# Kernel optimization log

Measured on AMD Instinct MI355X. Metric: run time of the kernel, lower is better.

## Reference

```python
import jax, jax.numpy as jnp
import numpy as np

VOCAB = 21
EPS = 1e-5


def rmsnorm(x, w):
    return x * jax.lax.rsqrt(jnp.mean(x * x, axis=-1, keepdims=True) + EPS) * w


def mamba_layer(h, in_w, conv_w, conv_b, xp_w, dtp_w, dtp_b, A_log, Dp, out_w):
    # h: (B, L, D)
    Bsz, L, _ = h.shape
    di, dc = conv_w.shape
    n = A_log.shape[-1]
    r = dtp_w.shape[-1]
    xz = jnp.einsum('bld,ed->ble', h, in_w)          # (B, L, 2*di)
    xi, z = jnp.split(xz, 2, axis=-1)
    # causal depthwise conv of width dc
    xp = jnp.pad(xi, ((0, 0), (dc - 1, 0), (0, 0)))
    xc = conv_b + sum(xp[:, k:k + L, :] * conv_w[:, k] for k in range(dc))
    xc = jax.nn.silu(xc)                              # (B, L, di)
    dbc = jnp.einsum('bld,ed->ble', xc, xp_w)         # (B, L, r+2n)
    dt, Bm, Cm = dbc[..., :r], dbc[..., r:r + n], dbc[..., r + n:]
    dt = jax.nn.softplus(jnp.einsum('blr,dr->bld', dt, dtp_w) + dtp_b)  # (B, L, di)
    A = -jnp.exp(A_log)                               # (di, n)

    def step(hst, inp):
        x_t, dt_t, B_t, C_t = inp                     # (B,di),(B,di),(B,n),(B,n)
        dA = jnp.exp(dt_t[..., None] * A)             # (B, di, n)
        hst = dA * hst + (dt_t * x_t)[..., None] * B_t[:, None, :]
        y_t = jnp.einsum('bdn,bn->bd', hst, C_t)
        return hst, y_t

    h0 = jnp.zeros((Bsz, di, n), dtype=h.dtype)
    xs = (xc.swapaxes(0, 1), dt.swapaxes(0, 1), Bm.swapaxes(0, 1), Cm.swapaxes(0, 1))
    _, ys = jax.lax.scan(step, h0, xs)
    y = ys.swapaxes(0, 1) + xc * Dp                   # skip term D*x
    y = y * jax.nn.silu(z)                            # gate
    return jnp.einsum('bld,ed->ble', y, out_w)


def setup_inputs() -> dict:
    key = jax.random.key(0)
    B, L, D = 4, 1024, 512
    n_layers, n, dc, expand = 2, 16, 3, 2
    di = expand * D
    r = (D + 15) // 16  # dt_rank = ceil(d_model/16) = 32
    ks = jax.random.split(key, 12)
    f32 = jnp.float32
    inp = {}
    inp['x'] = jax.random.randint(ks[0], (B, L), 0, VOCAB)
    inp['emb'] = 0.02 * jax.random.normal(ks[1], (VOCAB, D), f32)
    inp['norm_w'] = jnp.ones((n_layers, D), f32)
    inp['in_proj_w'] = (D ** -0.5) * jax.random.normal(ks[2], (n_layers, 2 * di, D), f32)
    inp['conv_w'] = (dc ** -0.5) * jax.random.normal(ks[3], (n_layers, di, dc), f32)
    inp['conv_b'] = jnp.zeros((n_layers, di), f32)
    inp['x_proj_w'] = (di ** -0.5) * jax.random.normal(ks[4], (n_layers, r + 2 * n, di), f32)
    inp['dt_proj_w'] = (r ** -0.5) * jax.random.normal(ks[5], (n_layers, di, r), f32)
    inp['dt_proj_b'] = jax.random.uniform(ks[6], (n_layers, di), f32, minval=-4.0, maxval=-1.0)
    inp['A_log'] = jnp.log(jnp.broadcast_to(jnp.arange(1, n + 1, dtype=f32), (n_layers, di, n)))
    inp['D_param'] = jnp.ones((n_layers, di), f32)
    inp['out_proj_w'] = (di ** -0.5) * jax.random.normal(ks[7], (n_layers, D, di), f32)
    inp['fc_w'] = (D ** -0.5) * jax.random.normal(ks[8], (2, D), f32)
    inp['fc_b'] = jnp.zeros((2,), f32)
    return inp


def reference(x, emb, norm_w, in_proj_w, conv_w, conv_b, x_proj_w, dt_proj_w,
              dt_proj_b, A_log, D_param, out_proj_w, fc_w, fc_b):
    h = emb[x].astype(jnp.float32)                    # (B, L, D)
    n_layers = norm_w.shape[0]
    for l in range(n_layers):
        h = rmsnorm(
            mamba_layer(h, in_proj_w[l], conv_w[l], conv_b[l], x_proj_w[l],
                        dt_proj_w[l], dt_proj_b[l], A_log[l], D_param[l],
                        out_proj_w[l]),
            norm_w[l])
    pooled = jnp.mean(h, axis=1)                      # global_pool=True
    out = jnp.tanh(pooled)                            # dropout is identity at eval
    return out @ fc_w.T + fc_b                        # (B, 2)
```

## Files before the change

### kernel.cpp

```cpp
#include <hip/hip_runtime.h>
#include <math.h>

constexpr int Bsz = 4, Lseq = 1024, Dmodel = 512, NLAYERS = 2;
constexpr int DI = 1024, NST = 16, RNK = 32;
constexpr int BLQ = Bsz * Lseq;
constexpr int NCH = 32, CLEN = 32;

typedef __attribute__((ext_vector_type(8))) short short8v;
typedef __attribute__((ext_vector_type(8))) unsigned short ushort8v;
typedef __attribute__((ext_vector_type(4))) float f32x4;
typedef unsigned short ushort;

__device__ inline ushort bf16_rne(float v) {
  unsigned u = __float_as_uint(v);
  u += 0x7FFFu + ((u >> 16) & 1u);
  return (ushort)(u >> 16);
}
__device__ inline float bf2f(ushort u) {
  return __uint_as_float(((unsigned)u) << 16);
}
__device__ inline size_t frag_off(int row, int k, int KT) {
  int kt = k >> 6, kk = (k >> 5) & 1, k8 = (k >> 3) & 3;
  int lanei = (row & 15) | (k8 << 4), msub = (row >> 4) & 7, rt = row >> 7;
  return ((((size_t)(rt * KT + kt) * 2 + kk) * 8 + msub) * 64 + lanei) * 8;
}
#define GLDS(gp, lp) __builtin_amdgcn_global_load_lds( \
    (const __attribute__((address_space(1))) void*)(gp), \
    (__attribute__((address_space(3))) void*)(lp), 16, 0, 0)

__global__ __launch_bounds__(256) void embcvt_kernel(
    const int* __restrict__ x, const float* __restrict__ emb,
    const float* __restrict__ in_w, const float* __restrict__ xp_w,
    const float* __restrict__ out_w,
    ushort* __restrict__ Af,
    ushort* __restrict__ WIh, ushort* __restrict__ WIl,
    ushort* __restrict__ XPh, ushort* __restrict__ XPl,
    ushort* __restrict__ WOh)
{
  int blk = blockIdx.x;
  if (blk < 1024) {
    int i = blk * 256 + threadIdx.x;
    int row = i >> 6, k = (i & 63) * 8;
    int tok = x[row];
    const float* src = &emb[(size_t)tok * Dmodel + k];
    float4 v0 = *reinterpret_cast<const float4*>(src);
    float4 v1 = *reinterpret_cast<const float4*>(src + 4);
    float xs[8] = {v0.x, v0.y, v0.z, v0.w, v1.x, v1.y, v1.z, v1.w};
    ushort hv[8];
#pragma unroll
    for (int e = 0; e < 8; ++e) hv[e] = bf16_rne(xs[e]);
    *reinterpret_cast<ushort8v*>(&Af[frag_off(row, k, 8)]) =
        *reinterpret_cast<ushort8v*>(hv);
    return;
  }
  const float* src; ushort *dh, *dl; size_t doff; bool wantlo = true;
  if (blk < 2048) {
    int u = (blk - 1024) * 256 + threadIdx.x;
    int l = u >> 17, rem = u & 131071;
    int row = rem >> 6, k = (rem & 63) * 8;
    src = in_w + (size_t)l * 2048 * 512 + (size_t)row * 512 + k;
    size_t base = (size_t)l * 2048 * 512;
    dh = WIh + base; dl = WIl + base; doff = frag_off(row, k, 8);
  } else if (blk < 2112) {
    int u = (blk - 2048) * 256 + threadIdx.x;
    int l = u >> 13, rem = u & 8191;
    int row = rem >> 7, k = (rem & 127) * 8;
    src = xp_w + (size_t)l * 64 * 1024 + (size_t)row * 1024 + k;
    size_t base = (size_t)l * 131072;
    dh = XPh + base; dl = XPl + base; doff = frag_off(row, k, 16);
  } else {
    int u = (blk - 2112) * 256 + threadIdx.x;
    int l = u >> 16, rem = u & 65535;
    int row = rem >> 7, k = (rem & 127) * 8;
    src = out_w + (size_t)l * 512 * 1024 + (size_t)row * 1024 + k;
    size_t base = (size_t)l * 512 * 1024;
    dh = WOh + base; dl = nullptr; doff = frag_off(row, k, 16); wantlo = false;
  }
  float4 v0 = *reinterpret_cast<const float4*>(src);
  float4 v1 = *reinterpret_cast<const float4*>(src + 4);
  float xs[8] = {v0.x, v0.y, v0.z, v0.w, v1.x, v1.y, v1.z, v1.w};
  ushort hs[8], ls[8];
#pragma unroll
  for (int j = 0; j < 8; ++j) {
    unsigned u = __float_as_uint(xs[j]);
    float hf = __uint_as_float(u & 0xFFFF0000u);
    float r = xs[j] - hf;
    hs[j] = (ushort)(u >> 16);
    ls[j] = (ushort)(__float_as_uint(r) >> 16);
  }
  *reinterpret_cast<ushort8v*>(&dh[doff]) = *reinterpret_cast<ushort8v*>(hs);
  if (wantlo)
    *reinterpret_cast<ushort8v*>(&dl[doff]) = *reinterpret_cast<ushort8v*>(ls);
}

__global__ __launch_bounds__(256) void gemm_in_mfma(
    const ushort* __restrict__ Ah,
    const ushort* __restrict__ Bh, const ushort* __restrict__ Bl,
    ushort* __restrict__ C)
{
  extern __shared__ ushort smu[];
  constexpr int AOFF = 0, BHOFF = 4096, BLOFF = 20480;
  const int tid = threadIdx.x, lane = tid & 63, wid = tid >> 6;
  const int bn = blockIdx.x, bm = blockIdx.y;
  const int bm0 = bm * 64;
  const int rtA = bm0 >> 7, half = (bm0 >> 6) & 1;
  f32x4 acc[4][4];
#pragma unroll
  for (int i = 0; i < 4; ++i)
#pragma unroll
    for (int j = 0; j < 4; ++j) acc[i][j] = (f32x4){0.f, 0.f, 0.f, 0.f};
  const int rtB = wid >> 1;
  const int nsub = (wid & 1) * 4;

  for (int kt = 0; kt < 8; ++kt) {
    if (wid == 0) {
      const ushort* cb = Ah + ((size_t)(rtA * 8 + kt)) * 8192;
#pragma unroll
      for (int kk = 0; kk < 2; ++kk)
#pragma unroll
        for (int m = 0; m < 4; ++m)
          GLDS(cb + (kk * 8 + half * 4 + m) * 512 + lane * 8,
               smu + AOFF + (kk * 4 + m) * 512);
    } else if (wid == 1) {
#pragma unroll
      for (int rt = 0; rt < 2; ++rt) {
        const ushort* cb = Bh + ((size_t)((bn * 2 + rt) * 8 + kt)) * 8192;
#pragma unroll
        for (int i = 0; i < 16; ++i)
          GLDS(cb + i * 512 + lane * 8, smu + BHOFF + rt * 8192 + i * 512);
      }
    } else if (wid == 2) {
#pragma unroll
      for (int rt = 0; rt < 2; ++rt) {
        const ushort* cb = Bl + ((size_t)((bn * 2 + rt) * 8 + kt)) * 8192;
#pragma unroll
        for (int i = 0; i < 16; ++i)
          GLDS(cb + i * 512 + lane * 8, smu + BLOFF + rt * 8192 + i * 512);
      }
    }
    __syncthreads();
#pragma unroll
    for (int kk = 0; kk < 2; ++kk) {
      short8v a[4], b[4];
#pragma unroll
      for (int i = 0; i < 4; ++i)
        a[i] = *reinterpret_cast<const short8v*>(&smu[AOFF + ((kk * 4 + i) * 64 + lane) * 8]);
#pragma unroll
      for (int j = 0; j < 4; ++j)
        b[j] = *reinterpret_cast<const short8v*>(
            &smu[BHOFF + rtB * 8192 + ((kk * 8 + nsub + j) * 64 + lane) * 8]);
#pragma unroll
      for (int ms = 0; ms < 4; ++ms)
#pragma unroll
        for (int ns = 0; ns < 4; ++ns)
          acc[ms][ns] = __builtin_amdgcn_mfma_f32_16x16x32_bf16(a[ms], b[ns], acc[ms][ns], 0, 0, 0);
#pragma unroll
      for (int j = 0; j < 4; ++j)
        b[j] = *reinterpret_cast<const short8v*>(
            &smu[BLOFF + rtB * 8192 + ((kk * 8 + nsub + j) * 64 + lane) * 8]);
#pragma unroll
      for (int ms = 0; ms < 4; ++ms)
#pragma unroll
        for (int ns = 0; ns < 4; ++ns)
          acc[ms][ns] = __builtin_amdgcn_mfma_f32_16x16x32_bf16(a[ms], b[ns], acc[ms][ns], 0, 0, 0);
    }
    __syncthreads();
  }
  const int cr = lane >> 4, cc = lane & 15;
#pragma unroll
  for (int ms = 0; ms < 4; ++ms) {
    int row0 = bm0 + ms * 16 + cr * 4;
#pragma unroll
    for (int ns = 0; ns < 4; ++ns) {
      int col = bn * 256 + wid * 64 + ns * 16 + cc;
#pragma unroll
      for (int r = 0; r < 4; ++r)
        C[(size_t)(row0 + r) * 2048 + col] = bf16_rne(acc[ms][ns][r]);
    }
  }
}

__global__ __launch_bounds__(256) void gemm_out_mfma(
    const ushort* __restrict__ Ah, const ushort* __restrict__ Bh,
    float* __restrict__ P)
{
  constexpr int ASZ = 8192;
  __shared__ ushort lds[2 * ASZ];
  const int tid = threadIdx.x, lane = tid & 63, wid = tid >> 6;
  const int wm = wid >> 1, wn = wid & 1;
  const int bm = blockIdx.y, bn = blockIdx.x, z = blockIdx.z;
  f32x4 acc[4][4];
#pragma unroll
  for (int i = 0; i < 4; ++i)
#pragma unroll
    for (int j = 0; j < 4; ++j) acc[i][j] = (f32x4){0.f, 0.f, 0.f, 0.f};
  const int msel = wm * 4, nsel = wn * 4;
  for (int kt = z * 4; kt < z * 4 + 4; ++kt) {
    if (wid == 0) {
      const ushort* cb = Ah + ((size_t)(bm * 16 + kt)) * 8192;
#pragma unroll
      for (int i = 0; i < 16; ++i)
        GLDS(cb + i * 512 + lane * 8, lds + i * 512);
    } else if (wid == 1) {
      const ushort* cb = Bh + ((size_t)(bn * 16 + kt)) * 8192;
#pragma unroll
      for (int i = 0; i < 16; ++i)
        GLDS(cb + i * 512 + lane * 8, lds + ASZ + i * 512);
    }
    __syncthreads();
#pragma unroll
    for (int kk = 0; kk < 2; ++kk) {
      short8v a[4], b[4];
#pragma unroll
      for (int i = 0; i < 4; ++i) {
        a[i] = *reinterpret_cast<const short8v*>(&lds[((kk * 8 + msel + i) * 64 + lane) * 8]);
        b[i] = *reinterpret_cast<const short8v*>(&lds[ASZ + ((kk * 8 + nsel + i) * 64 + lane) * 8]);
      }
#pragma unroll
      for (int ms = 0; ms < 4; ++ms)
#pragma unroll
        for (int ns = 0; ns < 4; ++ns)
          acc[ms][ns] = __builtin_amdgcn_mfma_f32_16x16x32_bf16(a[ms], b[ns], acc[ms][ns], 0, 0, 0);
    }
    __syncthreads();
  }
  float* Pz = P + (size_t)z * BLQ * Dmodel;
  const int cr = lane >> 4, cc = lane & 15;
#pragma unroll
  for (int ms = 0; ms < 4; ++ms) {
    int row0 = bm * 128 + (msel + ms) * 16 + cr * 4;
#pragma unroll
    for (int ns = 0; ns < 4; ++ns) {
      int col = bn * 128 + (nsel + ns) * 16 + cc;
#pragma unroll
      for (int r = 0; r < 4; ++r)
        Pz[(size_t)(row0 + r) * Dmodel + col] = acc[ms][ns][r];
    }
  }
}

__global__ __launch_bounds__(256) void convxp_kernel(
    const ushort* __restrict__ XZb, const float* __restrict__ cw,
    const float* __restrict__ cb,
    const ushort* __restrict__ XPh, const ushort* __restrict__ XPl,
    float* __restrict__ XC, float* __restrict__ P)
{
  constexpr int XZOFF = 0;
  constexpr int AOFF  = 1312;
  constexpr int BHOFF = 2336;
  constexpr int BLOFF = 6432;
  __shared__ ushort smu[10528];
  const int tid = threadIdx.x, lane = tid & 63, wid = tid >> 6;
  const int cr = lane >> 4, cc = lane & 15;
  const int bm0 = blockIdx.x * 16;
  const int z = blockIdx.y;
  const int batchbase = bm0 & ~(Lseq - 1);
  f32x4 acc = (f32x4){0.f, 0.f, 0.f, 0.f};

  for (int kt = z * 4; kt < z * 4 + 4; ++kt) {
    const int kcol0 = kt * 64;
    if (wid < 2) {
#pragma unroll
      for (int i = 0; i < 2; ++i) {
        int u = tid + i * 128;
        if (u < 144) {
          int r = u >> 3, c8 = u & 7;
          int grow = bm0 - 2 + r;
          ushort8v v = {};
          if (grow >= batchbase)
            v = *reinterpret_cast<const ushort8v*>(
                &XZb[(size_t)grow * 2048 + kcol0 + c8 * 8]);
          *reinterpret_cast<ushort8v*>(&smu[XZOFF + r * 72 + c8 * 8]) = v;
        }
      }
    } else {
      const ushort* src = ((wid == 2) ? XPh : XPl) + (size_t)kt * 8192 + lane * 8;
      int dst0 = (wid == 2) ? BHOFF : BLOFF;
#pragma unroll
      for (int i = 0; i < 8; ++i) {
        int sidx = (i >> 2) * 8 + (i & 3);
        GLDS(src + sidx * 512, smu + dst0 + i * 512);
      }
    }
    __syncthreads();
    if (tid < 128) {
      int row = tid >> 3, c8 = tid & 7;
      int d0 = kcol0 + c8 * 8;
      ushort8v cur = *reinterpret_cast<ushort8v*>(&smu[XZOFF + (row + 2) * 72 + c8 * 8]);
      ushort8v pm1 = *reinterpret_cast<ushort8v*>(&smu[XZOFF + (row + 1) * 72 + c8 * 8]);
      ushort8v pm2 = *reinterpret_cast<ushort8v*>(&smu[XZOFF + (row + 0) * 72 + c8 * 8]);
      float wv[24], bv[8];
#pragma unroll
      for (int q = 0; q < 6; ++q)
        *reinterpret_cast<float4*>(&wv[q * 4]) =
            *reinterpret_cast<const float4*>(&cw[d0 * 3 + q * 4]);
      *reinterpret_cast<float4*>(&bv[0]) = *reinterpret_cast<const float4*>(&cb[d0]);
      *reinterpret_cast<float4*>(&bv[4]) = *reinterpret_cast<const float4*>(&cb[d0 + 4]);
      float os[8]; ushort hv[8];
#pragma unroll
      for (int e = 0; e < 8; ++e) {
        float a = bv[e];
        a = fmaf(bf2f(pm2[e]), wv[e * 3 + 0], a);
        a = fmaf(bf2f(pm1[e]), wv[e * 3 + 1], a);
        a = fmaf(bf2f(cur[e]), wv[e * 3 + 2], a);
        float s = a / (1.f + __expf(-a));
        os[e] = s; hv[e] = bf16_rne(s);
      }
      float* op = &XC[(size_t)(bm0 + row) * DI + d0];
      *reinterpret_cast<float4*>(op) = *reinterpret_cast<float4*>(&os[0]);
      *reinterpret_cast<float4*>(op + 4) = *reinterpret_cast<float4*>(&os[4]);
      int kk = c8 >> 2, k8 = c8 & 3;
      int idx = (kk * 64 + (row | (k8 << 4))) ^ k8;
      *reinterpret_cast<ushort8v*>(&smu[AOFF + idx * 8]) =
          *reinterpret_cast<ushort8v*>(hv);
    }
    __syncthreads();
#pragma unroll
    for (int kk = 0; kk < 2; ++kk) {
      int aidx = (kk * 64 + lane) ^ ((lane >> 4) & 3);
      short8v a = *reinterpret_cast<const short8v*>(&smu[AOFF + aidx * 8]);
      short8v bh = *reinterpret_cast<const short8v*>(&smu[BHOFF + ((kk * 4 + wid) * 64 + lane) * 8]);
      short8v bl = *reinterpret_cast<const short8v*>(&smu[BLOFF + ((kk * 4 + wid) * 64 + lane) * 8]);
      acc = __builtin_amdgcn_mfma_f32_16x16x32_bf16(a, bh, acc, 0, 0, 0);
      acc = __builtin_amdgcn_mfma_f32_16x16x32_bf16(a, bl, acc, 0, 0, 0);
    }
    __syncthreads();
  }
  float* Pz = P + (size_t)z * BLQ * 64;
#pragma unroll
  for (int r = 0; r < 4; ++r)
    Pz[(size_t)(bm0 + cr * 4 + r) * 64 + wid * 16 + cc] = acc[r];
}

__global__ __launch_bounds__(256) void xpost_kernel(
    const float* __restrict__ P, const float* __restrict__ dtw,
    const float* __restrict__ dtb, float* __restrict__ DTb,
    float* __restrict__ BCc)
{
  const int tid = threadIdx.x;
  const size_t SL = (size_t)BLQ * 64;
  if (blockIdx.y == 16) {
    int i0 = blockIdx.x * 4096 + tid;
#pragma unroll
    for (int i = 0; i < 16; ++i) {
      int idx = i0 + i * 256;
      int bt = idx >> 5, n = idx & 31;
      size_t g = (size_t)bt * 64 + 32 + n;
      BCc[idx] = (P[g] + P[SL + g]) + (P[2 * SL + g] + P[3 * SL + g]);
    }
    return;
  }
  const int dg = blockIdx.y, bm0 = blockIdx.x * 128;
  __shared__ float db[128][33];
  __shared__ float wt[64][33];
#pragma unroll
  for (int i = 0; i < 16; ++i) {
    int e = tid + i * 256;
    int r = e >> 5, c = e & 31;
    size_t g = (size_t)(bm0 + r) * 64 + c;
    db[r][c] = (P[g] + P[SL + g]) + (P[2 * SL + g] + P[3 * SL + g]);
  }
#pragma unroll
  for (int i = 0; i < 8; ++i) {
    int e = tid + i * 256;
    int r = e >> 5, c = e & 31;
    wt[r][c] = dtw[(size_t)(dg * 64 + r) * 32 + c];
  }
  __syncthreads();
  const int d_loc = tid & 63, wv = tid >> 6;
  const float bias = dtb[dg * 64 + d_loc];
#pragma unroll 4
  for (int i = 0; i < 32; ++i) {
    int r = wv + i * 4;
    float dot = 0.f;
#pragma unroll
    for (int c = 0; c < 32; ++c) dot = fmaf(db[r][c], wt[d_loc][c], dot);
    float v = dot + bias;
    DTb[(size_t)(bm0 + r) * DI + dg * 64 + d_loc] =
        (v > 15.f) ? v : log1pf(__expf(v));
  }
}

__global__ __launch_bounds__(256) void scan_p1_kernel(
    const float* __restrict__ DTb, const float* __restrict__ XC,
    const float* __restrict__ BCc, const float* __restrict__ Alog,
    float* __restrict__ HEND, float* __restrict__ DSUM)
{
  const int d = blockIdx.x * 256 + threadIdx.x;
  const int c = blockIdx.y, b = blockIdx.z;
  const int t0 = b * Lseq + c * CLEN;
  __shared__ float Bs[CLEN][16];
#pragma unroll
  for (int i = 0; i < 2; ++i) {
    int e = threadIdx.x + i * 256;
    Bs[e >> 4][e & 15] = BCc[(size_t)(t0 + (e >> 4)) * 32 + (e & 15)];
  }
  float An[16];
#pragma unroll
  for (int j = 0; j < 4; ++j) {
    float4 a = *reinterpret_cast<const float4*>(&Alog[d * 16 + j * 4]);
    An[j * 4 + 0] = -__expf(a.x); An[j * 4 + 1] = -__expf(a.y);
    An[j * 4 + 2] = -__expf(a.z); An[j * 4 + 3] = -__expf(a.w);
  }
  __syncthreads();
  float h[16] = {};
  float S = 0.f;
  for (int t = 0; t < CLEN; ++t) {
    size_t g = (size_t)(t0 + t) * DI + d;
    float dt = DTb[g], xc = XC[g];
    S += dt;
    float dtxc = dt * xc;
#pragma unroll
    for (int n = 0; n < 16; ++n)
      h[n] = fmaf(__expf(An[n] * dt), h[n], dtxc * Bs[t][n]);
  }
  size_t hb = ((size_t)(b * NCH + c) * DI + d) * 16;
#pragma unroll
  for (int j = 0; j < 4; ++j)
    *reinterpret_cast<float4*>(&HEND[hb + j * 4]) =
        *reinterpret_cast<float4*>(&h[j * 4]);
  DSUM[(size_t)(b * NCH + c) * DI + d] = S;
}

__global__ __launch_bounds__(256) void scan_p2_kernel(
    float* __restrict__ HEND, const float* __restrict__ DSUM,
    const float* __restrict__ Alog)
{
  int id = blockIdx.x * 256 + threadIdx.x;
  int n = id & 15, d = (id >> 4) & (DI - 1), b = id >> 14;
  float An = -__expf(Alog[d * 16 + n]);
  float hg = 0.f;
  for (int c = 0; c < NCH; ++c) {
    size_t hi = ((size_t)(b * NCH + c) * DI + d) * 16 + n;
    float hl = HEND[hi];
    float Dc = DSUM[(size_t)(b * NCH + c) * DI + d];
    HEND[hi] = hg;
    hg = fmaf(__expf(An * Dc), hg, hl);
  }
}

__global__ __launch_bounds__(256) void scan_p3_kernel(
    const float* __restrict__ XC, const float* __restrict__ DTb,
    const float* __restrict__ BCc, const ushort* __restrict__ XZb,
    const float* __restrict__ HEND, const float* __restrict__ Alog,
    const float* __restrict__ Dp, ushort* __restrict__ Af)
{
  const int tid = threadIdx.x;
  const int dg = blockIdx.x, c = blockIdx.y, b = blockIdx.z;
  const int d = dg * 256 + tid;
  const int t0 = b * Lseq + c * CLEN;
  __shared__ float BC[CLEN][32];
  __shared__ float ys[CLEN][264];
#pragma unroll
  for (int i = 0; i < 4; ++i) {
    int e = tid + i * 256;
    BC[e >> 5][e & 31] = BCc[(size_t)(t0 + (e >> 5)) * 32 + (e & 31)];
  }
  float An[16], h[16];
  size_t hb = ((size_t)(b * NCH + c) * DI + d) * 16;
#pragma unroll
  for (int j = 0; j < 4; ++j) {
    float4 a = *reinterpret_cast<const float4*>(&Alog[d * 16 + j * 4]);
    An[j * 4 + 0] = -__expf(a.x); An[j * 4 + 1] = -__expf(a.y);
    An[j * 4 + 2] = -__expf(a.z); An[j * 4 + 3] = -__expf(a.w);
    *reinterpret_cast<float4*>(&h[j * 4]) =
        *reinterpret_cast<const float4*>(&HEND[hb + j * 4]);
  }
  float Dpv = Dp[d];
  __syncthreads();
  for (int t = 0; t < CLEN; ++t) {
    size_t g = (size_t)(t0 + t) * DI + d;
    float dt = DTb[g], xc = XC[g];
    float z = bf2f(XZb[(size_t)(t0 + t) * (2 * DI) + DI + d]);
    float dtxc = dt * xc;
    float y = 0.f;
#pragma unroll
    for (int n = 0; n < 16; ++n) {
      h[n] = fmaf(__expf(An[n] * dt), h[n], dtxc * BC[t][n]);
      y = fmaf(h[n], BC[t][16 + n], y);
    }
    float sil = z / (1.f + __expf(-z));
    ys[t][tid] = (y + xc * Dpv) * sil;
  }
  __syncthreads();
#pragma unroll
  for (int i = 0; i < 4; ++i) {
    int u = tid + i * 256;
    int tt = u >> 5, j8 = u & 31;
    int row = t0 + tt;
    int kg = dg * 256 + j8 * 8;
    ushort hv[8];
#pragma unroll
    for (int e = 0; e < 8; ++e) hv[e] = bf16_rne(ys[tt][j8 * 8 + e]);
    *reinterpret_cast<ushort8v*>(&Af[frag_off(row, kg, 16)]) =
        *reinterpret_cast<ushort8v*>(hv);
  }
}

template<int LAST>
__global__ __launch_bounds__(256) void rmsnorm_kernel(const float* __restrict__ X,
    const float* __restrict__ W, ushort* __restrict__ Af, float* __restrict__ PP) {
  __shared__ float pr[4][512];
  int w = threadIdx.x >> 6, lane = threadIdx.x & 63;
  int row = blockIdx.x * 4 + w;
  int k = lane * 8;
  const size_t SL = (size_t)BLQ * Dmodel;
  size_t idx = (size_t)row * Dmodel + k;
  float vs[8];
#pragma unroll
  for (int h = 0; h < 2; ++h) {
    float4 a = *reinterpret_cast<const float4*>(&X[idx + h * 4]);
    float4 b = *reinterpret_cast<const float4*>(&X[SL + idx + h * 4]);
    float4 c = *reinterpret_cast<const float4*>(&X[2 * SL + idx + h * 4]);
    float4 d = *reinterpret_cast<const float4*>(&X[3 * SL + idx + h * 4]);
    vs[h * 4 + 0] = (a.x + b.x) + (c.x + d.x);
    vs[h * 4 + 1] = (a.y + b.y) + (c.y + d.y);
    vs[h * 4 + 2] = (a.z + b.z) + (c.z + d.z);
    vs[h * 4 + 3] = (a.w + b.w) + (c.w + d.w);
  }
  float ss = 0.f;
#pragma unroll
  for (int e = 0; e < 8; ++e) ss = fmaf(vs[e], vs[e], ss);
#pragma unroll
  for (int o = 32; o >= 1; o >>= 1) ss += __shfl_xor(ss, o);
  float sc = rsqrtf(ss * (1.f / Dmodel) + 1e-5f);
  const float* wp = W + k;
  float4 w0 = *reinterpret_cast<const float4*>(wp);
  float4 w1 = *reinterpret_cast<const float4*>(wp + 4);
  float wsv[8] = {w0.x, w0.y, w0.z, w0.w, w1.x, w1.y, w1.z, w1.w};
  float os[8];
#pragma unroll
  for (int e = 0; e < 8; ++e) os[e] = vs[e] * sc * wsv[e];
  if (LAST == 0) {
    ushort hv[8];
#pragma unroll
    for (int e = 0; e < 8; ++e) hv[e] = bf16_rne(os[e]);
    *reinterpret_cast<ushort8v*>(&Af[frag_off(row, k, 8)]) =
        *reinterpret_cast<ushort8v*>(hv);
  } else {
#pragma unroll
    for (int e = 0; e < 8; ++e) pr[w][k + e] = os[e];
    __syncthreads();
#pragma unroll
    for (int i = 0; i < 2; ++i) {
      int d = threadIdx.x + i * 256;
      PP[(size_t)d * 1024 + blockIdx.x] =
          (pr[0][d] + pr[1][d]) + (pr[2][d] + pr[3][d]);
    }
  }
}

__global__ __launch_bounds__(256) void pool_head_kernel(
    const float* __restrict__ PP, const float* __restrict__ fcw,
    const float* __restrict__ fcb, float* __restrict__ out) {
  int b = blockIdx.x >> 1, j = blockIdx.x & 1;
  int tid = threadIdx.x;
  float s = 0.f;
  for (int d = tid; d < Dmodel; d += 256) {
    const float* pp = PP + (size_t)d * 1024 + b * 256;
    float p = 0.f;
#pragma unroll 8
    for (int blk = 0; blk < 256; ++blk) p += pp[blk];
    s += tanhf(p * (1.f / Lseq)) * fcw[j * Dmodel + d];
  }
#pragma unroll
  for (int o = 32; o >= 1; o >>= 1) s += __shfl_xor(s, o);
  __shared__ float w[4];
  if ((tid & 63) == 0) w[tid >> 6] = s;
  __syncthreads();
  if (tid == 0) out[b * 2 + j] = w[0] + w[1] + w[2] + w[3] + fcb[j];
}

extern "C" void kernel_launch(void* const* d_in, const int* in_sizes, int n_in,
                              void* d_out, int out_size, void* d_ws, size_t ws_size,
                              hipStream_t stream) {
  const int*   x      = (const int*)d_in[0];
  const float* emb    = (const float*)d_in[1];
  const float* norm_w = (const float*)d_in[2];
  const float* in_w   = (const float*)d_in[3];
  const float* conv_w = (const float*)d_in[4];
  const float* conv_b = (const float*)d_in[5];
  const float* xp_w   = (const float*)d_in[6];
  const float* dtp_w  = (const float*)d_in[7];
  const float* dtp_b  = (const float*)d_in[8];
  const float* A_log  = (const float*)d_in[9];
  const float* Dp     = (const float*)d_in[10];
  const float* out_w  = (const float*)d_in[11];
  const float* fc_w   = (const float*)d_in[12];
  const float* fc_b   = (const float*)d_in[13];
  float* out = (float*)d_out;

  char* p = (char*)d_ws;
  auto alloc = [&](size_t bytes) { char* r = p; p += (bytes + 255) & ~255ull; return r; };
  ushort* XZb  = (ushort*)alloc((size_t)BLQ * 2 * DI * 2);
  float*  XC   = (float*) alloc((size_t)BLQ * DI * 4);
  float*  DTb  = (float*) alloc((size_t)BLQ * DI * 4);
  float*  BCc  = (float*) alloc((size_t)BLQ * 32 * 4);
  float*  DBCP = (float*) alloc((size_t)4 * BLQ * 64 * 4);
  float*  HEND = (float*) alloc((size_t)Bsz * NCH * DI * 16 * 4);
  float*  DSUM = (float*) alloc((size_t)Bsz * NCH * DI * 4);
  float*  H2P  = (float*) alloc((size_t)4 * BLQ * Dmodel * 4);
  float*  PP   = (float*) alloc((size_t)Dmodel * 1024 * 4);
  ushort* AhI  = (ushort*)alloc((size_t)BLQ * Dmodel * 2);
  ushort* AhO  = (ushort*)alloc((size_t)BLQ * DI * 2);
  ushort* WIh  = (ushort*)alloc((size_t)2 * 2048 * 512 * 2);
  ushort* WIl  = (ushort*)alloc((size_t)2 * 2048 * 512 * 2);
  ushort* XPh  = (ushort*)alloc((size_t)2 * 131072 * 2);
  ushort* XPl  = (ushort*)alloc((size_t)2 * 131072 * 2);
  ushort* WOh  = (ushort*)alloc((size_t)2 * 512 * 1024 * 2);

  embcvt_kernel<<<2624, 256, 0, stream>>>(x, emb, in_w, xp_w, out_w,
      AhI, WIh, WIl, XPh, XPl, WOh);

  for (int l = 0; l < NLAYERS; ++l) {
    const float* cw  = conv_w + (size_t)l * DI * 3;
    const float* cb  = conv_b + (size_t)l * DI;
    const float* dtw = dtp_w + (size_t)l * DI * RNK;
    const float* dtb = dtp_b + (size_t)l * DI;
    const float* Al  = A_log + (size_t)l * DI * NST;
    const float* dpl = Dp    + (size_t)l * DI;
    const float* nw  = norm_w + (size_t)l * Dmodel;
    const ushort* wih = WIh + (size_t)l * 2048 * 512;
    const ushort* wil = WIl + (size_t)l * 2048 * 512;
    const ushort* xph = XPh + (size_t)l * 131072;
    const ushort* xpl = XPl + (size_t)l * 131072;
    const ushort* woh = WOh + (size_t)l * 512 * 1024;

    gemm_in_mfma<<<dim3(8, 64), 256, 73728, stream>>>(AhI, wih, wil, XZb);

    convxp_kernel<<<dim3(BLQ / 16, 4), 256, 0, stream>>>(XZb, cw, cb, xph, xpl,
        XC, DBCP);

    xpost_kernel<<<dim3(32, 17), 256, 0, stream>>>(DBCP, dtw, dtb, DTb, BCc);

    scan_p1_kernel<<<dim3(DI / 256, NCH, Bsz), 256, 0, stream>>>(
        DTb, XC, BCc, Al, HEND, DSUM);
    scan_p2_kernel<<<Bsz * DI * NST / 256, 256, 0, stream>>>(HEND, DSUM, Al);
    scan_p3_kernel<<<dim3(DI / 256, NCH, Bsz), 256, 0, stream>>>(
        XC, DTb, BCc, XZb, HEND, Al, dpl, AhO);

    gemm_out_mfma<<<dim3(4, 32, 4), 256, 0, stream>>>(AhO, woh, H2P);

    if (l == NLAYERS - 1)
      rmsnorm_kernel<1><<<BLQ / 4, 256, 0, stream>>>(H2P, nw, nullptr, PP);
    else
      rmsnorm_kernel<0><<<BLQ / 4, 256, 0, stream>>>(H2P, nw, AhI, nullptr);
  }

  pool_head_kernel<<<2 * Bsz, 256, 0, stream>>>(PP, fc_w, fc_b, out);
}
```

Measured before the change: 286.3 us.

## Fold chunk-prefix scan into scan_p3 and halve split-K partitions

Removes the scan_p2 kernel. Each scan_p3 block now recomputes its chunk's starting state by serially combining the HEND/DSUM values of all earlier chunks, which saves a launch and a global write-back but adds redundant work that grows with chunk index. Separately, the split-K factor for the x_proj and out_proj GEMMs drops from 4 to 2. That halves the partial buffers and the reduction reads in xpost and rmsnorm, at the cost of fewer blocks and longer K loops per block.

```diff
diff --git a/kernel.cpp b/kernel.cpp
--- a/kernel.cpp
+++ b/kernel.cpp
@@ -195,7 +195,7 @@
 #pragma unroll
     for (int j = 0; j < 4; ++j) acc[i][j] = (f32x4){0.f, 0.f, 0.f, 0.f};
   const int msel = wm * 4, nsel = wn * 4;
-  for (int kt = z * 4; kt < z * 4 + 4; ++kt) {
+  for (int kt = z * 8; kt < z * 8 + 8; ++kt) {
     if (wid == 0) {
       const ushort* cb = Ah + ((size_t)(bm * 16 + kt)) * 8192;
 #pragma unroll
@@ -257,7 +257,7 @@
   const int batchbase = bm0 & ~(Lseq - 1);
   f32x4 acc = (f32x4){0.f, 0.f, 0.f, 0.f};
 
-  for (int kt = z * 4; kt < z * 4 + 4; ++kt) {
+  for (int kt = z * 8; kt < z * 8 + 8; ++kt) {
     const int kcol0 = kt * 64;
     if (wid < 2) {
 #pragma unroll
@@ -346,7 +346,7 @@
       int idx = i0 + i * 256;
       int bt = idx >> 5, n = idx & 31;
       size_t g = (size_t)bt * 64 + 32 + n;
-      BCc[idx] = (P[g] + P[SL + g]) + (P[2 * SL + g] + P[3 * SL + g]);
+      BCc[idx] = P[g] + P[SL + g];
     }
     return;
   }
@@ -358,7 +358,7 @@
     int e = tid + i * 256;
     int r = e >> 5, c = e & 31;
     size_t g = (size_t)(bm0 + r) * 64 + c;
-    db[r][c] = (P[g] + P[SL + g]) + (P[2 * SL + g] + P[3 * SL + g]);
+    db[r][c] = P[g] + P[SL + g];
   }
 #pragma unroll
   for (int i = 0; i < 8; ++i) {
@@ -422,28 +422,12 @@
   DSUM[(size_t)(b * NCH + c) * DI + d] = S;
 }
 
-__global__ __launch_bounds__(256) void scan_p2_kernel(
-    float* __restrict__ HEND, const float* __restrict__ DSUM,
-    const float* __restrict__ Alog)
-{
-  int id = blockIdx.x * 256 + threadIdx.x;
-  int n = id & 15, d = (id >> 4) & (DI - 1), b = id >> 14;
-  float An = -__expf(Alog[d * 16 + n]);
-  float hg = 0.f;
-  for (int c = 0; c < NCH; ++c) {
-    size_t hi = ((size_t)(b * NCH + c) * DI + d) * 16 + n;
-    float hl = HEND[hi];
-    float Dc = DSUM[(size_t)(b * NCH + c) * DI + d];
-    HEND[hi] = hg;
-    hg = fmaf(__expf(An * Dc), hg, hl);
-  }
-}
-
 __global__ __launch_bounds__(256) void scan_p3_kernel(
     const float* __restrict__ XC, const float* __restrict__ DTb,
     const float* __restrict__ BCc, const ushort* __restrict__ XZb,
-    const float* __restrict__ HEND, const float* __restrict__ Alog,
-    const float* __restrict__ Dp, ushort* __restrict__ Af)
+    const float* __restrict__ HEND, const float* __restrict__ DSUM,
+    const float* __restrict__ Alog, const float* __restrict__ Dp,
+    ushort* __restrict__ Af)
 {
   const int tid = threadIdx.x;
   const int dg = blockIdx.x, c = blockIdx.y, b = blockIdx.z;
@@ -457,14 +441,24 @@
     BC[e >> 5][e & 31] = BCc[(size_t)(t0 + (e >> 5)) * 32 + (e & 31)];
   }
   float An[16], h[16];
-  size_t hb = ((size_t)(b * NCH + c) * DI + d) * 16;
 #pragma unroll
   for (int j = 0; j < 4; ++j) {
     float4 a = *reinterpret_cast<const float4*>(&Alog[d * 16 + j * 4]);
     An[j * 4 + 0] = -__expf(a.x); An[j * 4 + 1] = -__expf(a.y);
     An[j * 4 + 2] = -__expf(a.z); An[j * 4 + 3] = -__expf(a.w);
-    *reinterpret_cast<float4*>(&h[j * 4]) =
-        *reinterpret_cast<const float4*>(&HEND[hb + j * 4]);
+    h[j * 4 + 0] = 0.f; h[j * 4 + 1] = 0.f; h[j * 4 + 2] = 0.f; h[j * 4 + 3] = 0.f;
+  }
+  for (int j = 0; j < c; ++j) {
+    float Dc = DSUM[(size_t)(b * NCH + j) * DI + d];
+    size_t hb = ((size_t)(b * NCH + j) * DI + d) * 16;
+    float he[16];
+#pragma unroll
+    for (int q = 0; q < 4; ++q)
+      *reinterpret_cast<float4*>(&he[q * 4]) =
+          *reinterpret_cast<const float4*>(&HEND[hb + q * 4]);
+#pragma unroll
+    for (int n = 0; n < 16; ++n)
+      h[n] = fmaf(__expf(An[n] * Dc), h[n], he[n]);
   }
   float Dpv = Dp[d];
   __syncthreads();
@@ -511,12 +505,10 @@
   for (int h = 0; h < 2; ++h) {
     float4 a = *reinterpret_cast<const float4*>(&X[idx + h * 4]);
     float4 b = *reinterpret_cast<const float4*>(&X[SL + idx + h * 4]);
-    float4 c = *reinterpret_cast<const float4*>(&X[2 * SL + idx + h * 4]);
-    float4 d = *reinterpret_cast<const float4*>(&X[3 * SL + idx + h * 4]);
-    vs[h * 4 + 0] = (a.x + b.x) + (c.x + d.x);
-    vs[h * 4 + 1] = (a.y + b.y) + (c.y + d.y);
-    vs[h * 4 + 2] = (a.z + b.z) + (c.z + d.z);
-    vs[h * 4 + 3] = (a.w + b.w) + (c.w + d.w);
+    vs[h * 4 + 0] = a.x + b.x;
+    vs[h * 4 + 1] = a.y + b.y;
+    vs[h * 4 + 2] = a.z + b.z;
+    vs[h * 4 + 3] = a.w + b.w;
   }
   float ss = 0.f;
 #pragma unroll
@@ -596,10 +588,10 @@
   float*  XC   = (float*) alloc((size_t)BLQ * DI * 4);
   float*  DTb  = (float*) alloc((size_t)BLQ * DI * 4);
   float*  BCc  = (float*) alloc((size_t)BLQ * 32 * 4);
-  float*  DBCP = (float*) alloc((size_t)4 * BLQ * 64 * 4);
+  float*  DBCP = (float*) alloc((size_t)2 * BLQ * 64 * 4);
   float*  HEND = (float*) alloc((size_t)Bsz * NCH * DI * 16 * 4);
   float*  DSUM = (float*) alloc((size_t)Bsz * NCH * DI * 4);
-  float*  H2P  = (float*) alloc((size_t)4 * BLQ * Dmodel * 4);
+  float*  H2P  = (float*) alloc((size_t)2 * BLQ * Dmodel * 4);
   float*  PP   = (float*) alloc((size_t)Dmodel * 1024 * 4);
   ushort* AhI  = (ushort*)alloc((size_t)BLQ * Dmodel * 2);
   ushort* AhO  = (ushort*)alloc((size_t)BLQ * DI * 2);
@@ -628,18 +620,17 @@
 
     gemm_in_mfma<<<dim3(8, 64), 256, 73728, stream>>>(AhI, wih, wil, XZb);
 
-    convxp_kernel<<<dim3(BLQ / 16, 4), 256, 0, stream>>>(XZb, cw, cb, xph, xpl,
+    convxp_kernel<<<dim3(BLQ / 16, 2), 256, 0, stream>>>(XZb, cw, cb, xph, xpl,
         XC, DBCP);
 
     xpost_kernel<<<dim3(32, 17), 256, 0, stream>>>(DBCP, dtw, dtb, DTb, BCc);
 
     scan_p1_kernel<<<dim3(DI / 256, NCH, Bsz), 256, 0, stream>>>(
         DTb, XC, BCc, Al, HEND, DSUM);
-    scan_p2_kernel<<<Bsz * DI * NST / 256, 256, 0, stream>>>(HEND, DSUM, Al);
     scan_p3_kernel<<<dim3(DI / 256, NCH, Bsz), 256, 0, stream>>>(
-        XC, DTb, BCc, XZb, HEND, Al, dpl, AhO);
-
-    gemm_out_mfma<<<dim3(4, 32, 4), 256, 0, stream>>>(AhO, woh, H2P);
+        XC, DTb, BCc, XZb, HEND, DSUM, Al, dpl, AhO);
+
+    gemm_out_mfma<<<dim3(4, 32, 2), 256, 0, stream>>>(AhO, woh, H2P);
 
     if (l == NLAYERS - 1)
       rmsnorm_kernel<1><<<BLQ / 4, 256, 0, stream>>>(H2P, nw, nullptr, PP);
```

Measured after the change: 304.6 us. 1.06x slower.
